# Optimization experiments

Measured on AMD Instinct MI355X. Metric: run time of the kernel, lower is better.

## Reference

```python
import jax, jax.numpy as jnp
import numpy as np

N, S, E, H = 8, 1024, 1024, 16
DK = E // H

def setup_inputs() -> dict:
    key = jax.random.key(0)
    ks = jax.random.split(key, 10)
    s = 1.0 / np.sqrt(E)
    x = jax.random.normal(ks[0], (N, S, E), dtype=jnp.float32)
    attn_mask = jax.random.randint(ks[1], (N, S, S), 0, 2) == 1
    Wq = jax.random.normal(ks[2], (E, E), dtype=jnp.float32) * s
    Wk = jax.random.normal(ks[3], (E, E), dtype=jnp.float32) * s
    Wv = jax.random.normal(ks[4], (E, E), dtype=jnp.float32) * s
    Wo = jax.random.normal(ks[5], (E, E), dtype=jnp.float32) * s
    bq = jax.random.normal(ks[6], (E,), dtype=jnp.float32) * s
    bk = jax.random.normal(ks[7], (E,), dtype=jnp.float32) * s
    bv = jax.random.normal(ks[8], (E,), dtype=jnp.float32) * s
    bo = jax.random.normal(ks[9], (E,), dtype=jnp.float32) * s
    return {"x": x, "attn_mask": attn_mask, "Wq": Wq, "bq": bq, "Wk": Wk, "bk": bk,
            "Wv": Wv, "bv": bv, "Wo": Wo, "bo": bo}

def reference(x, attn_mask, Wq, bq, Wk, bk, Wv, bv, Wo, bo):
    n, s, e = x.shape
    # projections, split into heads: (N, H, S, DK)
    q = (x @ Wq + bq).reshape(n, s, H, DK).transpose(0, 2, 1, 3)
    k = (x @ Wk + bk).reshape(n, s, H, DK).transpose(0, 2, 1, 3)
    v = (x @ Wv + bv).reshape(n, s, H, DK).transpose(0, 2, 1, 3)
    logits = jnp.einsum("nhqd,nhkd->nhqk", q, k) / np.sqrt(DK).astype(np.float32)
    # mask==True positions are suppressed (masked_fill with -1e9)
    logits = jnp.where(attn_mask[:, None, :, :], jnp.float32(-1e9), logits)
    attn = jax.nn.softmax(logits, axis=-1)  # exp(log_softmax) == softmax
    o = jnp.einsum("nhqk,nhkd->nhqd", attn, v)
    o = o.transpose(0, 2, 1, 3).reshape(n, s, e)
    return o @ Wo + bo
```

## Files before the change

### kernel.cpp

```cpp
#include <hip/hip_runtime.h>
#include <hip/hip_bf16.h>

typedef unsigned short u16;
typedef unsigned int   u32;
typedef unsigned long long u64;

#define SEQ 1024
#define EMB 1024
#define NH  16
#define DKH 64

#define QSCALE 0.18033688f

typedef __attribute__((ext_vector_type(8))) short short8;
typedef __attribute__((ext_vector_type(4))) float floatx4;

__device__ __forceinline__ float b2f(u16 u) {
  return __uint_as_float(((u32)u) << 16);
}
__device__ __forceinline__ u16 f2b(float f) {
  u32 u = __float_as_uint(f);
  u32 r = u + 0x7fffu + ((u >> 16) & 1u);
  return (u16)(r >> 16);
}

__device__ __forceinline__ void glds16(const u16* g, u16* l) {
  __builtin_amdgcn_global_load_lds(
      (const __attribute__((address_space(1))) u32*)g,
      (__attribute__((address_space(3))) u32*)l, 16, 0, 0);
}

__global__ __launch_bounds__(256) void probe_inputs(const u32* __restrict__ A,
                                                    const u32* __restrict__ B,
                                                    int* __restrict__ flags) {
  __shared__ int mA, mB, mBig, xB16;
  if (threadIdx.x == 0) { mA = 0; mB = 0; mBig = 0; xB16 = 0; }
  __syncthreads();
  int la = 0, lb = 0;
  for (int i = threadIdx.x; i < 4096; i += 256) {
    if ((A[i] & 0xFEFEFEFEu) == 0) la++;
    if ((B[i] & 0xFEFEFEFEu) == 0) lb++;
  }
  atomicAdd(&mA, la); atomicAdd(&mB, lb);
  __syncthreads();
  const int xIsB = (mA > mB) ? 1 : 0;
  const u32* X = xIsB ? B : A;
  const u32* M = xIsB ? A : B;
  int big = 0, cnt = 0;
  for (int i = threadIdx.x; i < 4096; i += 256)
    if (M[i] > 1u) big = 1;
  for (int i = threadIdx.x; i < 2048; i += 256) {
    u16 v = (u16)(X[i] & 0xffffu);
    int e = (v >> 7) & 0xFF;
    if (e >= 110 && e <= 135) cnt++;
  }
  if (big) atomicOr(&mBig, 1);
  atomicAdd(&xB16, cnt);
  __syncthreads();
  if (threadIdx.x == 0) {
    flags[0] = xIsB;
    flags[1] = (xB16 > 1500) ? 1 : 0;
    flags[2] = mBig;
  }
}

__global__ __launch_bounds__(256) void convert_x(const void* __restrict__ bigA,
                                                 const void* __restrict__ bigB,
                                                 const int* __restrict__ flags,
                                                 u16* __restrict__ out) {
  const void* x = flags[0] ? bigB : bigA;
  int i = (blockIdx.x * 256 + threadIdx.x) * 4;
  if (flags[1]) {
    *(ushort4*)(out + i) = *(const ushort4*)((const u16*)x + i);
  } else {
    float4 v = *(const float4*)((const float*)x + i);
    ushort4 o;
    o.x = f2b(v.x); o.y = f2b(v.y); o.z = f2b(v.z); o.w = f2b(v.w);
    *(ushort4*)(out + i) = o;
  }
}

__global__ __launch_bounds__(256) void build_maskbits(const void* __restrict__ bigA,
                                                      const void* __restrict__ bigB,
                                                      const int* __restrict__ flags,
                                                      u32* __restrict__ out) {
  const void* mask = flags[0] ? bigA : bigB;
  const int mbyte = flags[2];
  const int t = threadIdx.x;
  const int lane = t & 63, w = t >> 6;
  const u64 base0 = (u64)blockIdx.x * 8192;
#pragma unroll 4
  for (int k = 0; k < 32; k++) {
    u64 idx = base0 + k * 256 + t;
    int v;
    if (mbyte) v = ((const unsigned char*)mask)[idx] == 0;
    else       v = ((const u32*)mask)[idx] == 0;
    u64 b = __ballot(v);
    if (lane == 0) {
      u64 wbase = (base0 + k * 256 + w * 64) >> 5;
      out[wbase]     = (u32)b;
      out[wbase + 1] = (u32)(b >> 32);
    }
  }
}

__global__ __launch_bounds__(256) void transpose_convert_w4(
    const void* __restrict__ w0, const void* __restrict__ w1,
    const void* __restrict__ w2, const void* __restrict__ w3,
    u16* __restrict__ outQKV, u16* __restrict__ outO,
    const int* __restrict__ flags) {
  __shared__ float tile[32][33];
  const int z = blockIdx.z;
  const void* in = (z == 0) ? w0 : (z == 1) ? w1 : (z == 2) ? w2 : w3;
  u16* out = (z < 3) ? (outQKV + (u64)z * EMB * EMB) : outO;
  const float scale = (z == 0) ? QSCALE : 1.0f;
  const int amode = flags[1];
  const int tx = threadIdx.x & 31;
  const int ty = threadIdx.x >> 5;
  const int bx = blockIdx.x * 32, by = blockIdx.y * 32;
  if (amode) {
    const u16* inb = (const u16*)in;
#pragma unroll
    for (int r = ty; r < 32; r += 8)
      tile[r][tx] = b2f(inb[(u64)(by + r) * EMB + bx + tx]);
  } else {
    const float* inf = (const float*)in;
#pragma unroll
    for (int r = ty; r < 32; r += 8)
      tile[r][tx] = inf[(u64)(by + r) * EMB + bx + tx];
  }
  __syncthreads();
#pragma unroll
  for (int r = ty; r < 32; r += 8)
    out[(u64)(bx + r) * EMB + by + tx] = f2b(tile[tx][r] * scale);
}

__global__ __launch_bounds__(256) void convert_biases(const void* b0, const void* b1,
                                                      const void* b2, const void* b3,
                                                      float* __restrict__ out,
                                                      const int* __restrict__ flags) {
  const void* ptrs[4] = {b0, b1, b2, b3};
  const void* p = ptrs[blockIdx.x];
  const float scale = (blockIdx.x == 0) ? QSCALE : 1.0f;
  const int amode = flags[1];
  for (int i = threadIdx.x; i < 1024; i += 256) {
    float v = amode ? b2f(((const u16*)p)[i]) : ((const float*)p)[i];
    out[blockIdx.x * 1024 + i] = v * scale;
  }
}


template <int OUTMODE>
__device__ __forceinline__ void gemm_core(
    const u16* __restrict__ X, const u16* __restrict__ Wt,
    const float* __restrict__ bias,
    u16* __restrict__ Qg, u16* __restrict__ Kg, u16* __restrict__ Vt,
    float* __restrict__ outf, int row0) {
  __shared__ __align__(16) u16 lds[2][(256 + 128) * 64];
  const int t = threadIdx.x;
  const int lane = t & 63;
  const int w = t >> 6;
  const int wr = w >> 1, wc = w & 1;
  const int l15 = lane & 15, l4 = lane >> 4;
  const int bM = blockIdx.x * 256, bN = blockIdx.y * 128;
  const int r7 = l15 & 7;
  const int cA = (l4 ^ r7) << 3;
  const int cB = (l4 ^ r7 ^ 4) << 3;

  floatx4 acc[4][4];
#pragma unroll
  for (int i = 0; i < 4; i++)
#pragma unroll
    for (int j = 0; j < 4; j++)
      acc[i][j] = (floatx4){0.f, 0.f, 0.f, 0.f};

  const int srow = w * 8 + (lane >> 3);
  const int schk = ((lane & 7) ^ (lane >> 3)) << 3;
  const u16* Ap = X + (u64)(row0 + bM + srow) * EMB + schk;
  const u16* Bp = Wt + (u64)(bN + srow) * EMB + schk;
  u16* Ad0 = &lds[0][w * 512];
  u16* Bd0 = &lds[0][16384 + w * 512];
  u16* Ad1 = &lds[1][w * 512];
  u16* Bd1 = &lds[1][16384 + w * 512];

  auto stage = [&](u16* Ad, u16* Bd, int k0) {
    glds16(Ap + k0, Ad);
    glds16(Ap + k0 + 64 * EMB, Ad + 4096);
    glds16(Ap + k0 + 128 * EMB, Ad + 8192);
    glds16(Ap + k0 + 192 * EMB, Ad + 12288);
    glds16(Bp + k0, Bd);
    glds16(Bp + k0 + 64 * EMB, Bd + 4096);
  };

  auto compute = [&](const u16* __restrict__ Ab, const u16* __restrict__ Bb) {
    short8 bf[4][2];
#pragma unroll
    for (int n = 0; n < 4; n++) {
      const int gr = (wc * 64 + n * 16 + l15) * 64;
      bf[n][0] = *(const short8*)(&Bb[gr + cA]);
      bf[n][1] = *(const short8*)(&Bb[gr + cB]);
    }
#pragma unroll
    for (int mh = 0; mh < 2; mh++) {
      short8 af[2][2];
#pragma unroll
      for (int m = 0; m < 2; m++) {
        const int fr = (wr * 64 + mh * 32 + m * 16 + l15) * 64;
        af[m][0] = *(const short8*)(&Ab[fr + cA]);
        af[m][1] = *(const short8*)(&Ab[fr + cB]);
      }
      __builtin_amdgcn_s_setprio(1);
#pragma unroll
      for (int m = 0; m < 2; m++)
#pragma unroll
        for (int n = 0; n < 4; n++) {
          acc[mh * 2 + m][n] = __builtin_amdgcn_mfma_f32_16x16x32_bf16(
              af[m][0], bf[n][0], acc[mh * 2 + m][n], 0, 0, 0);
          acc[mh * 2 + m][n] = __builtin_amdgcn_mfma_f32_16x16x32_bf16(
              af[m][1], bf[n][1], acc[mh * 2 + m][n], 0, 0, 0);
        }
      __builtin_amdgcn_s_setprio(0);
    }
  };

  stage(Ad0, Bd0, 0);
  for (int k0 = 0; k0 < EMB; k0 += 128) {
    stage(Ad1, Bd1, k0 + 64);
    asm volatile("s_waitcnt vmcnt(6)" ::: "memory");
    asm volatile("s_barrier" ::: "memory");
    compute(&lds[0][0], &lds[0][16384]);
    asm volatile("s_barrier" ::: "memory");
    if (k0 + 128 < EMB) {
      stage(Ad0, Bd0, k0 + 128);
      asm volatile("s_waitcnt vmcnt(6)" ::: "memory");
    } else {
      asm volatile("s_waitcnt vmcnt(0)" ::: "memory");
    }
    asm volatile("s_barrier" ::: "memory");
    compute(&lds[1][0], &lds[1][16384]);
    asm volatile("s_barrier" ::: "memory");
  }

  if (OUTMODE == 0) {
    const int sec = bN >> 10;
    if (sec < 2) {
      u16* outp = (sec == 0) ? Qg : Kg;
#pragma unroll
      for (int n = 0; n < 4; n++) {
        int col = bN + wc * 64 + n * 16 + l15;
        float bv = bias[col];
        int colh = col & 1023;
        int h = colh >> 6, d = colh & 63;
#pragma unroll
        for (int mt = 0; mt < 4; mt++) {
#pragma unroll
          for (int r = 0; r < 4; r++) {
            int row = bM + wr * 64 + mt * 16 + l4 * 4 + r;
            float v = acc[mt][n][r] + bv;
            int nb = row >> 10, s = row & 1023;
            outp[((u64)((nb * NH + h) * SEQ + s)) * DKH + d] = f2b(v);
          }
        }
      }
    } else {
      u16* ldt = &lds[0][0];
#pragma unroll
      for (int n = 0; n < 4; n++) {
        const int dl = wc * 64 + n * 16 + l15;
        const float bv = bias[bN + dl];
#pragma unroll
        for (int mt = 0; mt < 4; mt++) {
          const int sb = wr * 64 + mt * 16 + l4 * 4;
          const int sp = sb ^ ((dl & 7) << 3);
          u32 w0 = (u32)f2b(acc[mt][n][0] + bv) |
                   ((u32)f2b(acc[mt][n][1] + bv) << 16);
          u32 w1 = (u32)f2b(acc[mt][n][2] + bv) |
                   ((u32)f2b(acc[mt][n][3] + bv) << 16);
          *(u32*)(&ldt[dl * 256 + sp])     = w0;
          *(u32*)(&ldt[dl * 256 + sp + 2]) = w1;
        }
      }
      __syncthreads();
      const int d  = t >> 2;
      const int sq = (t & 3) * 64;
      const int arow = row0 + bM;
      const int nb = arow >> 10, s0 = arow & 1023;
      const int h = ((bN & 1023) >> 6) + (d >> 6);
      u16* vout = Vt + (u64)(nb * NH + h) * SEQ * DKH +
                  (u64)(d & 63) * SEQ + s0 + sq;
#pragma unroll
      for (int c = 0; c < 8; c++) {
        const int sc = sq + c * 8;
        const int scs = sc ^ ((d & 7) << 3);
        *(uint4*)(vout + c * 8) = *(const uint4*)(&ldt[d * 256 + scs]);
      }
    }
  } else {
#pragma unroll
    for (int n = 0; n < 4; n++) {
      int col = bN + wc * 64 + n * 16 + l15;
      float bv = bias[col];
#pragma unroll
      for (int mt = 0; mt < 4; mt++) {
#pragma unroll
        for (int r = 0; r < 4; r++) {
          int row = bM + wr * 64 + mt * 16 + l4 * 4 + r;
          outf[(u64)row * EMB + col] = acc[mt][n][r] + bv;
        }
      }
    }
  }
}

__global__ __launch_bounds__(512, 2) void gemm_qkv(
    const u16* __restrict__ X, const u16* __restrict__ Wt,
    const float* __restrict__ bias,
    u16* __restrict__ Qg, u16* __restrict__ Kg, u16* __restrict__ Vt,
    int row0) {
  gemm_core<0>(X, Wt, bias, Qg, Kg, Vt, nullptr, row0);
}

__global__ __launch_bounds__(512, 2) void gemm_out(
    const u16* __restrict__ X, const u16* __restrict__ Wt,
    const float* __restrict__ bias, float* __restrict__ out) {
  gemm_core<1>(X, Wt, bias, nullptr, nullptr, nullptr, out, 0);
}

__global__ __launch_bounds__(512, 4) void attn_mfma(
    const u16* __restrict__ Q, const u16* __restrict__ K,
    const u16* __restrict__ Vt, const u32* __restrict__ maskbits,
    int b0, u16* __restrict__ ctx) {
  __shared__ __align__(16) u16 Ks[2][64 * 64];
  __shared__ __align__(16) u16 Vs[64 * 64];
  __shared__ __align__(16) u16 Ps[256 * 64];

  const int t = threadIdx.x;
  const int lane = t & 63, w = t >> 6;
  const int l15 = lane & 15, l4 = lane >> 4;
  const int bid = blockIdx.x;
  const int h = bid & 15;
  const int qt = (bid >> 4) & 3;
  const int n = bid >> 6;
  const int nh = n * NH + h;
  const int q0 = qt * 256;
  const u64 hoff = (u64)nh * SEQ * DKH;

  const int r7 = l15 & 7;
  const int cA = (l4 ^ r7) << 3;
  const int cB = (l4 ^ r7 ^ 4) << 3;

  const int rt = w * 8 + (lane >> 3);
  const int chk = ((lane & 7) ^ (lane >> 3)) << 3;
  const u16* Kp = K + hoff + (u64)rt * DKH + chk;
  const u16* Vp = Vt + hoff + (u64)rt * SEQ + chk;
  const int ldsO = w * 512;

  short8 qf[2][2];
  {
    const u16* qpA = Q + hoff + (u64)(q0 + w * 32 + l15) * DKH + l4 * 8;
    qf[0][0] = *(const short8*)(qpA);
    qf[0][1] = *(const short8*)(qpA + 32);
    const u16* qpB = qpA + 16 * DKH;
    qf[1][0] = *(const short8*)(qpB);
    qf[1][1] = *(const short8*)(qpB + 32);
  }

  short8 ones;
#pragma unroll
  for (int e = 0; e < 8; e++) ones[e] = (short)0x3F80;

  floatx4 o[2][4];
#pragma unroll
  for (int s = 0; s < 2; s++)
#pragma unroll
    for (int j = 0; j < 4; j++) o[s][j] = (floatx4){0.f, 0.f, 0.f, 0.f};
  floatx4 osum[2];
  osum[0] = (floatx4){0.f, 0.f, 0.f, 0.f};
  osum[1] = (floatx4){0.f, 0.f, 0.f, 0.f};

  const u64 mrow0 = ((u64)((b0 + n) * SEQ + q0 + w * 32 + l15)) * 32;
  const u64 mrow1 = mrow0 + 16 * 32;
  const int pq0 = w * 32 + l15;
  const int pq1 = pq0 + 16;
  const int pc0 = (l4 * 4) ^ (r7 << 3);

  glds16(Kp, &Ks[0][ldsO]);
  glds16(Vp, &Vs[ldsO]);
  __syncthreads();

  int cur = 0;
  for (int kc = 0; kc < SEQ; kc += 64) {
    if (kc > 0) glds16(Vp + kc, &Vs[ldsO]);
    const int havek = (kc + 64 < SEQ);
    if (havek) glds16(Kp + (kc + 64) * DKH, &Ks[cur ^ 1][ldsO]);

    const u64 mb0 = *(const u64*)(maskbits + mrow0 + (kc >> 5));
    const u64 mb1 = *(const u64*)(maskbits + mrow1 + (kc >> 5));
    const u16* Kc = &Ks[cur][0];

    __builtin_amdgcn_s_setprio(1);
#pragma unroll
    for (int j = 0; j < 4; j++) {
      const int rb = (j * 16 + l15) * 64;
      short8 kb0 = *(const short8*)(&Kc[rb + cA]);
      short8 kb1 = *(const short8*)(&Kc[rb + cB]);
      floatx4 s0 = (floatx4){0.f, 0.f, 0.f, 0.f};
      floatx4 s1 = (floatx4){0.f, 0.f, 0.f, 0.f};
      s0 = __builtin_amdgcn_mfma_f32_16x16x32_bf16(kb0, qf[0][0], s0, 0, 0, 0);
      s0 = __builtin_amdgcn_mfma_f32_16x16x32_bf16(kb1, qf[0][1], s0, 0, 0, 0);
      s1 = __builtin_amdgcn_mfma_f32_16x16x32_bf16(kb0, qf[1][0], s1, 0, 0, 0);
      s1 = __builtin_amdgcn_mfma_f32_16x16x32_bf16(kb1, qf[1][1], s1, 0, 0, 0);

      const u32 mj0 = (u32)(mb0 >> (j * 16 + l4 * 4));
      const u32 mj1 = (u32)(mb1 >> (j * 16 + l4 * 4));
      float p00 = __uint_as_float(
          __float_as_uint(__builtin_amdgcn_exp2f(s0[0])) &
          (u32)__builtin_amdgcn_sbfe(mj0, 0, 1));
      float p01 = __uint_as_float(
          __float_as_uint(__builtin_amdgcn_exp2f(s0[1])) &
          (u32)__builtin_amdgcn_sbfe(mj0, 1, 1));
      float p02 = __uint_as_float(
          __float_as_uint(__builtin_amdgcn_exp2f(s0[2])) &
          (u32)__builtin_amdgcn_sbfe(mj0, 2, 1));
      float p03 = __uint_as_float(
          __float_as_uint(__builtin_amdgcn_exp2f(s0[3])) &
          (u32)__builtin_amdgcn_sbfe(mj0, 3, 1));
      float p10 = __uint_as_float(
          __float_as_uint(__builtin_amdgcn_exp2f(s1[0])) &
          (u32)__builtin_amdgcn_sbfe(mj1, 0, 1));
      float p11 = __uint_as_float(
          __float_as_uint(__builtin_amdgcn_exp2f(s1[1])) &
          (u32)__builtin_amdgcn_sbfe(mj1, 1, 1));
      float p12 = __uint_as_float(
          __float_as_uint(__builtin_amdgcn_exp2f(s1[2])) &
          (u32)__builtin_amdgcn_sbfe(mj1, 2, 1));
      float p13 = __uint_as_float(
          __float_as_uint(__builtin_amdgcn_exp2f(s1[3])) &
          (u32)__builtin_amdgcn_sbfe(mj1, 3, 1));

      uint2 pk0, pk1;
      asm("v_cvt_pk_bf16_f32 %0, %1, %2" : "=v"(pk0.x) : "v"(p00), "v"(p01));
      asm("v_cvt_pk_bf16_f32 %0, %1, %2" : "=v"(pk0.y) : "v"(p02), "v"(p03));
      asm("v_cvt_pk_bf16_f32 %0, %1, %2" : "=v"(pk1.x) : "v"(p10), "v"(p11));
      asm("v_cvt_pk_bf16_f32 %0, %1, %2" : "=v"(pk1.y) : "v"(p12), "v"(p13));
      const int pcol = (j * 16) ^ pc0;
      *(uint2*)(&Ps[pq0 * 64 + pcol]) = pk0;
      *(uint2*)(&Ps[pq1 * 64 + pcol]) = pk1;
    }

    if (havek) asm volatile("s_waitcnt vmcnt(1)" ::: "memory");
    else       asm volatile("s_waitcnt vmcnt(0)" ::: "memory");
    __builtin_amdgcn_s_barrier();

    short8 pa[2][2];
    pa[0][0] = *(const short8*)(&Ps[pq0 * 64 + cA]);
    pa[0][1] = *(const short8*)(&Ps[pq0 * 64 + cB]);
    pa[1][0] = *(const short8*)(&Ps[pq1 * 64 + cA]);
    pa[1][1] = *(const short8*)(&Ps[pq1 * 64 + cB]);
#pragma unroll
    for (int j = 0; j < 4; j++) {
      const int rb = (j * 16 + l15) * 64;
      short8 vb0 = *(const short8*)(&Vs[rb + cA]);
      short8 vb1 = *(const short8*)(&Vs[rb + cB]);
      o[0][j] = __builtin_amdgcn_mfma_f32_16x16x32_bf16(pa[0][0], vb0, o[0][j], 0, 0, 0);
      o[0][j] = __builtin_amdgcn_mfma_f32_16x16x32_bf16(pa[0][1], vb1, o[0][j], 0, 0, 0);
      o[1][j] = __builtin_amdgcn_mfma_f32_16x16x32_bf16(pa[1][0], vb0, o[1][j], 0, 0, 0);
      o[1][j] = __builtin_amdgcn_mfma_f32_16x16x32_bf16(pa[1][1], vb1, o[1][j], 0, 0, 0);
    }
    osum[0] = __builtin_amdgcn_mfma_f32_16x16x32_bf16(pa[0][0], ones, osum[0], 0, 0, 0);
    osum[0] = __builtin_amdgcn_mfma_f32_16x16x32_bf16(pa[0][1], ones, osum[0], 0, 0, 0);
    osum[1] = __builtin_amdgcn_mfma_f32_16x16x32_bf16(pa[1][0], ones, osum[1], 0, 0, 0);
    osum[1] = __builtin_amdgcn_mfma_f32_16x16x32_bf16(pa[1][1], ones, osum[1], 0, 0, 0);
    __builtin_amdgcn_s_setprio(0);

    __syncthreads();
    cur ^= 1;
  }

#pragma unroll
  for (int s = 0; s < 2; s++) {
#pragma unroll
    for (int r = 0; r < 4; r++) {
      float invr = 1.0f / fmaxf(osum[s][r], 1e-30f);
      int q = q0 + w * 32 + s * 16 + l4 * 4 + r;
      u64 base = ((u64)(n * SEQ + q)) * EMB + h * DKH + l15;
#pragma unroll
      for (int j = 0; j < 4; j++)
        ctx[base + j * 16] = f2b(o[s][j][r] * invr);
    }
  }
}

extern "C" void kernel_launch(void* const* d_in, const int* in_sizes, int n_in,
                              void* d_out, int out_size, void* d_ws, size_t ws_size,
                              hipStream_t stream) {
  int bigI[2] = {0, 1}, wI[4] = {2, 4, 6, 8}, bI[4] = {3, 5, 7, 9};
  int nb = 0, nw = 0, nbi = 0;
  for (int i = 0; i < n_in; i++) {
    if (in_sizes[i] == 8388608) { if (nb < 2) bigI[nb++] = i; }
    else if (in_sizes[i] == 1048576) { if (nw < 4) wI[nw++] = i; }
    else if (in_sizes[i] == 1024) { if (nbi < 4) bI[nbi++] = i; }
  }
  int oq = 0, ok = 1, ov = 2, oo = 3;
  if (nb == 2 && bigI[0] == 4 && bigI[1] == 9) { oq = 2; ok = 0; ov = 3; oo = 1; }

  const void* bigA = d_in[bigI[0]];
  const void* bigB = d_in[bigI[1]];
  const void* Wq = d_in[wI[oq]];
  const void* Wk = d_in[wI[ok]];
  const void* Wv = d_in[wI[ov]];
  const void* Wo = d_in[wI[oo]];
  const void* bq = d_in[bI[oq]];
  const void* bk = d_in[bI[ok]];
  const void* bv = d_in[bI[ov]];
  const void* bo = d_in[bI[oo]];

  char* ws = (char*)d_ws;
  u16* WtQKV = (u16*)ws;
  u16* WtO   = (u16*)(ws + (6ull << 20));
  float* biasf = (float*)(ws + (8ull << 20));
  int* flags = (int*)(ws + (8ull << 20) + 16384);
  u32* maskbits = (u32*)(ws + (8ull << 20) + 65536);
  u16* xb = (u16*)(ws + (10ull << 20));
  char* grp = ws + (26ull << 20);

  int G = 1;
  for (int g = 8; g >= 1; g >>= 1) {
    if (ws_size >= (26ull << 20) + (u64)g * (8ull << 20)) { G = g; break; }
  }
  const u64 gsz = (u64)G * (2ull << 20);
  u16* Qg = (u16*)grp;
  u16* Kg = (u16*)(grp + gsz);
  u16* ctx = (u16*)(grp + 2 * gsz);
  u16* Vt = (u16*)(grp + 3 * gsz);

  dim3 tb(256);

  probe_inputs<<<dim3(1), tb, 0, stream>>>((const u32*)bigA, (const u32*)bigB, flags);
  convert_x<<<dim3(8192), tb, 0, stream>>>(bigA, bigB, flags, xb);
  build_maskbits<<<dim3(1024), tb, 0, stream>>>(bigA, bigB, flags, maskbits);

  transpose_convert_w4<<<dim3(32, 32, 4), tb, 0, stream>>>(Wq, Wk, Wv, Wo, WtQKV, WtO, flags);
  convert_biases<<<dim3(4), tb, 0, stream>>>(bq, bk, bv, bo, biasf, flags);

  for (int b0 = 0; b0 < 8; b0 += G) {
    int row0 = b0 * 1024;
    gemm_qkv<<<dim3(4 * G, 24), dim3(512), 0, stream>>>(xb, WtQKV, biasf, Qg, Kg, Vt, row0);

    attn_mfma<<<dim3(G * 16 * 4), dim3(512), 0, stream>>>(Qg, Kg, Vt, maskbits, b0, ctx);

    gemm_out<<<dim3(4 * G, 8), dim3(512), 0, stream>>>(ctx, WtO, biasf + 3072,
                                                       (float*)d_out + (u64)row0 * EMB);
  }
}
```

Before: 304.4 us.

## Triple-buffer GEMM LDS and interleave prefetch loads with MFMA phases

Replaces the double-buffered K loop in the shared projection GEMM with a three-stage LDS ring, prefetching two tiles ahead. Each iteration splits its work into four MFMA phases separated by barriers, and the global-to-LDS loads for the next stage are spread across those phases. The intent is to hide global memory latency better and to keep MFMA issue dense while loads are in flight. In exchange it uses 50% more LDS, which can lower occupancy, and adds more barriers per iteration.

```diff
diff --git a/kernel.cpp b/kernel.cpp
--- a/kernel.cpp
+++ b/kernel.cpp
@@ -14,6 +14,8 @@
 
 typedef __attribute__((ext_vector_type(8))) short short8;
 typedef __attribute__((ext_vector_type(4))) float floatx4;
+
+#define MM(A, B, C) C = __builtin_amdgcn_mfma_f32_16x16x32_bf16(A, B, C, 0, 0, 0)
 
 __device__ __forceinline__ float b2f(u16 u) {
   return __uint_as_float(((u32)u) << 16);
@@ -150,13 +152,15 @@
 }
 
 
+#define LDSB 24576
+
 template <int OUTMODE>
 __device__ __forceinline__ void gemm_core(
     const u16* __restrict__ X, const u16* __restrict__ Wt,
     const float* __restrict__ bias,
     u16* __restrict__ Qg, u16* __restrict__ Kg, u16* __restrict__ Vt,
     float* __restrict__ outf, int row0) {
-  __shared__ __align__(16) u16 lds[2][(256 + 128) * 64];
+  __shared__ __align__(16) u16 lds[3 * LDSB];
   const int t = threadIdx.x;
   const int lane = t & 63;
   const int w = t >> 6;
@@ -178,67 +182,103 @@
   const int schk = ((lane & 7) ^ (lane >> 3)) << 3;
   const u16* Ap = X + (u64)(row0 + bM + srow) * EMB + schk;
   const u16* Bp = Wt + (u64)(bN + srow) * EMB + schk;
-  u16* Ad0 = &lds[0][w * 512];
-  u16* Bd0 = &lds[0][16384 + w * 512];
-  u16* Ad1 = &lds[1][w * 512];
-  u16* Bd1 = &lds[1][16384 + w * 512];
-
-  auto stage = [&](u16* Ad, u16* Bd, int k0) {
+  const int wo = w * 512;
+
+#pragma unroll
+  for (int b = 0; b < 2; b++) {
+    u16* Ad = lds + b * LDSB + wo;
+    u16* Bd = lds + b * LDSB + 16384 + wo;
+    const int k0 = b * 64;
     glds16(Ap + k0, Ad);
     glds16(Ap + k0 + 64 * EMB, Ad + 4096);
     glds16(Ap + k0 + 128 * EMB, Ad + 8192);
     glds16(Ap + k0 + 192 * EMB, Ad + 12288);
     glds16(Bp + k0, Bd);
     glds16(Bp + k0 + 64 * EMB, Bd + 4096);
-  };
-
-  auto compute = [&](const u16* __restrict__ Ab, const u16* __restrict__ Bb) {
-    short8 bf[4][2];
-#pragma unroll
-    for (int n = 0; n < 4; n++) {
-      const int gr = (wc * 64 + n * 16 + l15) * 64;
-      bf[n][0] = *(const short8*)(&Bb[gr + cA]);
-      bf[n][1] = *(const short8*)(&Bb[gr + cB]);
-    }
-#pragma unroll
-    for (int mh = 0; mh < 2; mh++) {
-      short8 af[2][2];
-#pragma unroll
-      for (int m = 0; m < 2; m++) {
-        const int fr = (wr * 64 + mh * 32 + m * 16 + l15) * 64;
-        af[m][0] = *(const short8*)(&Ab[fr + cA]);
-        af[m][1] = *(const short8*)(&Ab[fr + cB]);
-      }
-      __builtin_amdgcn_s_setprio(1);
-#pragma unroll
-      for (int m = 0; m < 2; m++)
-#pragma unroll
-        for (int n = 0; n < 4; n++) {
-          acc[mh * 2 + m][n] = __builtin_amdgcn_mfma_f32_16x16x32_bf16(
-              af[m][0], bf[n][0], acc[mh * 2 + m][n], 0, 0, 0);
-          acc[mh * 2 + m][n] = __builtin_amdgcn_mfma_f32_16x16x32_bf16(
-              af[m][1], bf[n][1], acc[mh * 2 + m][n], 0, 0, 0);
-        }
-      __builtin_amdgcn_s_setprio(0);
-    }
-  };
-
-  stage(Ad0, Bd0, 0);
-  for (int k0 = 0; k0 < EMB; k0 += 128) {
-    stage(Ad1, Bd1, k0 + 64);
-    asm volatile("s_waitcnt vmcnt(6)" ::: "memory");
-    asm volatile("s_barrier" ::: "memory");
-    compute(&lds[0][0], &lds[0][16384]);
-    asm volatile("s_barrier" ::: "memory");
-    if (k0 + 128 < EMB) {
-      stage(Ad0, Bd0, k0 + 128);
-      asm volatile("s_waitcnt vmcnt(6)" ::: "memory");
-    } else {
-      asm volatile("s_waitcnt vmcnt(0)" ::: "memory");
-    }
-    asm volatile("s_barrier" ::: "memory");
-    compute(&lds[1][0], &lds[1][16384]);
-    asm volatile("s_barrier" ::: "memory");
+  }
+  asm volatile("s_waitcnt vmcnt(6)" ::: "memory");
+  __builtin_amdgcn_s_barrier();
+
+  int cur = 0;
+#pragma unroll 1
+  for (int kt = 0; kt < 16; kt++) {
+    const u16* Ab = lds + cur * LDSB;
+    const u16* Bb = Ab + 16384;
+    const int nxb = (cur + 2 >= 3) ? (cur - 1) : (cur + 2);
+    u16* And = lds + nxb * LDSB + wo;
+    u16* Bnd = And + 16384;
+    const int kof = (kt + 2) * 64;
+    const bool pf = kt < 14;
+
+    short8 af[2][2], bf[4][2];
+    const int raA = (wr * 64 + l15) * 64;
+    const int rbB = (wc * 64 + l15) * 64;
+
+    af[0][0] = *(const short8*)&Ab[raA + cA];
+    af[0][1] = *(const short8*)&Ab[raA + cB];
+    af[1][0] = *(const short8*)&Ab[raA + 1024 + cA];
+    af[1][1] = *(const short8*)&Ab[raA + 1024 + cB];
+    bf[0][0] = *(const short8*)&Bb[rbB + cA];
+    bf[0][1] = *(const short8*)&Bb[rbB + cB];
+    bf[1][0] = *(const short8*)&Bb[rbB + 1024 + cA];
+    bf[1][1] = *(const short8*)&Bb[rbB + 1024 + cB];
+    if (pf) {
+      glds16(Ap + kof, And);
+      glds16(Ap + kof + 64 * EMB, And + 4096);
+    }
+    __builtin_amdgcn_s_barrier();
+    __builtin_amdgcn_s_setprio(1);
+    MM(af[0][0], bf[0][0], acc[0][0]); MM(af[0][1], bf[0][1], acc[0][0]);
+    MM(af[0][0], bf[1][0], acc[0][1]); MM(af[0][1], bf[1][1], acc[0][1]);
+    MM(af[1][0], bf[0][0], acc[1][0]); MM(af[1][1], bf[0][1], acc[1][0]);
+    MM(af[1][0], bf[1][0], acc[1][1]); MM(af[1][1], bf[1][1], acc[1][1]);
+    __builtin_amdgcn_s_setprio(0);
+    __builtin_amdgcn_s_barrier();
+
+    bf[2][0] = *(const short8*)&Bb[rbB + 2048 + cA];
+    bf[2][1] = *(const short8*)&Bb[rbB + 2048 + cB];
+    bf[3][0] = *(const short8*)&Bb[rbB + 3072 + cA];
+    bf[3][1] = *(const short8*)&Bb[rbB + 3072 + cB];
+    if (pf) {
+      glds16(Ap + kof + 128 * EMB, And + 8192);
+      glds16(Ap + kof + 192 * EMB, And + 12288);
+    }
+    __builtin_amdgcn_s_barrier();
+    __builtin_amdgcn_s_setprio(1);
+    MM(af[0][0], bf[2][0], acc[0][2]); MM(af[0][1], bf[2][1], acc[0][2]);
+    MM(af[0][0], bf[3][0], acc[0][3]); MM(af[0][1], bf[3][1], acc[0][3]);
+    MM(af[1][0], bf[2][0], acc[1][2]); MM(af[1][1], bf[2][1], acc[1][2]);
+    MM(af[1][0], bf[3][0], acc[1][3]); MM(af[1][1], bf[3][1], acc[1][3]);
+    __builtin_amdgcn_s_setprio(0);
+    __builtin_amdgcn_s_barrier();
+
+    af[0][0] = *(const short8*)&Ab[raA + 2048 + cA];
+    af[0][1] = *(const short8*)&Ab[raA + 2048 + cB];
+    af[1][0] = *(const short8*)&Ab[raA + 3072 + cA];
+    af[1][1] = *(const short8*)&Ab[raA + 3072 + cB];
+    if (pf) glds16(Bp + kof, Bnd);
+    __builtin_amdgcn_s_barrier();
+    __builtin_amdgcn_s_setprio(1);
+    MM(af[0][0], bf[2][0], acc[2][2]); MM(af[0][1], bf[2][1], acc[2][2]);
+    MM(af[0][0], bf[3][0], acc[2][3]); MM(af[0][1], bf[3][1], acc[2][3]);
+    MM(af[1][0], bf[2][0], acc[3][2]); MM(af[1][1], bf[2][1], acc[3][2]);
+    MM(af[1][0], bf[3][0], acc[3][3]); MM(af[1][1], bf[3][1], acc[3][3]);
+    __builtin_amdgcn_s_setprio(0);
+    __builtin_amdgcn_s_barrier();
+
+    if (pf) glds16(Bp + kof + 64 * EMB, Bnd + 4096);
+    __builtin_amdgcn_s_barrier();
+    __builtin_amdgcn_s_setprio(1);
+    MM(af[0][0], bf[0][0], acc[2][0]); MM(af[0][1], bf[0][1], acc[2][0]);
+    MM(af[0][0], bf[1][0], acc[2][1]); MM(af[0][1], bf[1][1], acc[2][1]);
+    MM(af[1][0], bf[0][0], acc[3][0]); MM(af[1][1], bf[0][1], acc[3][0]);
+    MM(af[1][0], bf[1][0], acc[3][1]); MM(af[1][1], bf[1][1], acc[3][1]);
+    __builtin_amdgcn_s_setprio(0);
+    if (kt < 14) asm volatile("s_waitcnt vmcnt(6)" ::: "memory");
+    else         asm volatile("s_waitcnt vmcnt(0)" ::: "memory");
+    __builtin_amdgcn_s_barrier();
+
+    cur = (cur == 2) ? 0 : cur + 1;
   }
 
   if (OUTMODE == 0) {
@@ -263,7 +303,7 @@
         }
       }
     } else {
-      u16* ldt = &lds[0][0];
+      u16* ldt = &lds[0];
 #pragma unroll
       for (int n = 0; n < 4; n++) {
         const int dl = wc * 64 + n * 16 + l15;
```

Result: no change. 309.0 us (+1.5%).

## Use 256x256 tiles with staggered interleaved prefetch in QKV projection GEMM

Applied to the files above, without the earlier changes.

Splits the QKV GEMM out of the shared template and gives it a 256x256 output tile per block (8 waves in a 2x4 layout, 8x4 accumulators per wave) instead of 256x128, halving the grid's N dimension. Global-to-LDS loads for the next k-tiles are spread across the four sub-steps of each k-iteration, with barriers between them, so loads overlap the MFMA work. The aim is more data reuse per LDS byte and fewer redundant A-tile reloads. The cost is higher register pressure from 128 accumulator floats and a fuller 128KB LDS buffer, which may lower occupancy. The V transpose epilogue is rewritten to match the larger tile.

```diff
diff --git a/kernel.cpp b/kernel.cpp
--- a/kernel.cpp
+++ b/kernel.cpp
@@ -14,6 +14,8 @@
 
 typedef __attribute__((ext_vector_type(8))) short short8;
 typedef __attribute__((ext_vector_type(4))) float floatx4;
+
+#define MM(A, B, C) C = __builtin_amdgcn_mfma_f32_16x16x32_bf16(A, B, C, 0, 0, 0)
 
 __device__ __forceinline__ float b2f(u16 u) {
   return __uint_as_float(((u32)u) << 16);
@@ -149,13 +151,171 @@
   }
 }
 
-
-template <int OUTMODE>
-__device__ __forceinline__ void gemm_core(
+__global__ __launch_bounds__(512, 2) void gemm_qkv(
     const u16* __restrict__ X, const u16* __restrict__ Wt,
     const float* __restrict__ bias,
     u16* __restrict__ Qg, u16* __restrict__ Kg, u16* __restrict__ Vt,
-    float* __restrict__ outf, int row0) {
+    int row0) {
+  __shared__ __align__(16) u16 lds[65536];
+  const int t = threadIdx.x;
+  const int lane = t & 63;
+  const int w = t >> 6;
+  const int wr = w >> 2, wc = w & 3;
+  const int l15 = lane & 15, l4 = lane >> 4;
+  const int bM = blockIdx.x * 256, bN = blockIdx.y * 256;
+  const int r7 = l15 & 7;
+  const int cA = (l4 ^ r7) << 3;
+  const int cB = (l4 ^ r7 ^ 4) << 3;
+
+  floatx4 acc[8][4];
+#pragma unroll
+  for (int i = 0; i < 8; i++)
+#pragma unroll
+    for (int j = 0; j < 4; j++)
+      acc[i][j] = (floatx4){0.f, 0.f, 0.f, 0.f};
+
+  const int srow = w * 8 + (lane >> 3);
+  const int schk = ((lane & 7) ^ (lane >> 3)) << 3;
+  const u16* Ap = X + (u64)(row0 + bM + srow) * EMB + schk;
+  const u16* Bp = Wt + (u64)(bN + srow) * EMB + schk;
+  const int wo = w * 512;
+
+#define STA(buf, g, kt) glds16(Ap + (g) * 64 * EMB + (kt) * 64, lds + (buf) * 32768 + (g) * 4096 + wo)
+#define STB(buf, g, kt) glds16(Bp + (g) * 64 * EMB + (kt) * 64, lds + (buf) * 32768 + 16384 + (g) * 4096 + wo)
+
+  STB(0, 0, 0); STB(0, 1, 0);
+  STB(0, 2, 0); STB(0, 3, 0);
+  STA(0, 0, 0); STA(0, 2, 0);
+  STA(0, 1, 0); STA(0, 3, 0);
+  STB(1, 0, 1); STB(1, 1, 1);
+  STB(1, 2, 1); STB(1, 3, 1);
+  STA(1, 0, 1); STA(1, 2, 1);
+  asm volatile("s_waitcnt vmcnt(6)" ::: "memory");
+  __builtin_amdgcn_s_barrier();
+
+#pragma unroll 1
+  for (int kt = 0; kt < 16; kt++) {
+    const int cur = kt & 1, nxt = cur ^ 1;
+    const u16* Ab = lds + cur * 32768;
+    const u16* Bb = Ab + 16384;
+    const int raA = (wr * 128 + l15) * 64;
+    const int rbB = (wc * 64 + l15) * 64;
+    short8 bf[4][2];
+    short8 af[2][2];
+
+    {
+#pragma unroll
+      for (int n = 0; n < 4; n++) {
+        bf[n][0] = *(const short8*)&Bb[rbB + n * 1024 + cA];
+        bf[n][1] = *(const short8*)&Bb[rbB + n * 1024 + cB];
+      }
+      af[0][0] = *(const short8*)&Ab[raA + cA];
+      af[0][1] = *(const short8*)&Ab[raA + cB];
+      af[1][0] = *(const short8*)&Ab[raA + 1024 + cA];
+      af[1][1] = *(const short8*)&Ab[raA + 1024 + cB];
+      if (kt + 1 < 16) { STA(nxt, 1, kt + 1); STA(nxt, 3, kt + 1); }
+      __builtin_amdgcn_s_barrier();
+      __builtin_amdgcn_s_setprio(1);
+#pragma unroll
+      for (int m = 0; m < 2; m++)
+#pragma unroll
+        for (int n = 0; n < 4; n++) {
+          MM(af[m][0], bf[n][0], acc[m][n]);
+          MM(af[m][1], bf[n][1], acc[m][n]);
+        }
+      __builtin_amdgcn_s_setprio(0);
+      __builtin_amdgcn_s_barrier();
+    }
+#pragma unroll
+    for (int q = 1; q < 4; q++) {
+      af[0][0] = *(const short8*)&Ab[raA + (2 * q) * 1024 + cA];
+      af[0][1] = *(const short8*)&Ab[raA + (2 * q) * 1024 + cB];
+      af[1][0] = *(const short8*)&Ab[raA + (2 * q + 1) * 1024 + cA];
+      af[1][1] = *(const short8*)&Ab[raA + (2 * q + 1) * 1024 + cB];
+      if (kt + 2 < 16) {
+        if (q == 1)      { STB(cur, 0, kt + 2); STB(cur, 1, kt + 2); }
+        else if (q == 2) { STB(cur, 2, kt + 2); STB(cur, 3, kt + 2); }
+        else             { STA(cur, 0, kt + 2); STA(cur, 2, kt + 2); }
+      }
+      __builtin_amdgcn_s_barrier();
+      __builtin_amdgcn_s_setprio(1);
+#pragma unroll
+      for (int m = 0; m < 2; m++)
+#pragma unroll
+        for (int n = 0; n < 4; n++) {
+          MM(af[m][0], bf[n][0], acc[2 * q + m][n]);
+          MM(af[m][1], bf[n][1], acc[2 * q + m][n]);
+        }
+      __builtin_amdgcn_s_setprio(0);
+      if (q == 3) {
+        if (kt < 14) asm volatile("s_waitcnt vmcnt(6)" ::: "memory");
+        else         asm volatile("s_waitcnt vmcnt(0)" ::: "memory");
+      }
+      __builtin_amdgcn_s_barrier();
+    }
+  }
+#undef STA
+#undef STB
+
+  const int sec = bN >> 10;
+  if (sec < 2) {
+    u16* outp = (sec == 0) ? Qg : Kg;
+#pragma unroll
+    for (int n = 0; n < 4; n++) {
+      int col = bN + wc * 64 + n * 16 + l15;
+      float bv = bias[col];
+      int colh = col & 1023;
+      int h = colh >> 6, d = colh & 63;
+#pragma unroll
+      for (int m = 0; m < 8; m++) {
+#pragma unroll
+        for (int r = 0; r < 4; r++) {
+          int row = bM + wr * 128 + m * 16 + l4 * 4 + r;
+          float v = acc[m][n][r] + bv;
+          int nb = row >> 10, s = row & 1023;
+          outp[((u64)((nb * NH + h) * SEQ + s)) * DKH + d] = f2b(v);
+        }
+      }
+    }
+  } else {
+    __syncthreads();
+    u16* ldt = &lds[0];
+#pragma unroll
+    for (int n = 0; n < 4; n++) {
+      const int dl = wc * 64 + n * 16 + l15;
+      const float bv = bias[bN + dl];
+#pragma unroll
+      for (int m = 0; m < 8; m++) {
+        const int sb = wr * 128 + m * 16 + l4 * 4;
+        const int sp = sb ^ ((dl & 7) << 3);
+        u32 w0 = (u32)f2b(acc[m][n][0] + bv) |
+                 ((u32)f2b(acc[m][n][1] + bv) << 16);
+        u32 w1 = (u32)f2b(acc[m][n][2] + bv) |
+                 ((u32)f2b(acc[m][n][3] + bv) << 16);
+        *(u32*)(&ldt[dl * 256 + sp])     = w0;
+        *(u32*)(&ldt[dl * 256 + sp + 2]) = w1;
+      }
+    }
+    __syncthreads();
+    const int d  = t >> 1;
+    const int sh = (t & 1) * 128;
+    const int arow = row0 + bM;
+    const int nb = arow >> 10, s0 = arow & 1023;
+    const int h = ((bN & 1023) >> 6) + (d >> 6);
+    u16* vout = Vt + (u64)(nb * NH + h) * SEQ * DKH +
+                (u64)(d & 63) * SEQ + s0 + sh;
+#pragma unroll
+    for (int c = 0; c < 16; c++) {
+      const int sc = sh + c * 8;
+      const int scs = sc ^ ((d & 7) << 3);
+      *(uint4*)(vout + c * 8) = *(const uint4*)(&ldt[d * 256 + scs]);
+    }
+  }
+}
+
+__global__ __launch_bounds__(512, 2) void gemm_out(
+    const u16* __restrict__ X, const u16* __restrict__ Wt,
+    const float* __restrict__ bias, float* __restrict__ out) {
   __shared__ __align__(16) u16 lds[2][(256 + 128) * 64];
   const int t = threadIdx.x;
   const int lane = t & 63;
@@ -176,7 +336,7 @@
 
   const int srow = w * 8 + (lane >> 3);
   const int schk = ((lane & 7) ^ (lane >> 3)) << 3;
-  const u16* Ap = X + (u64)(row0 + bM + srow) * EMB + schk;
+  const u16* Ap = X + (u64)(bM + srow) * EMB + schk;
   const u16* Bp = Wt + (u64)(bN + srow) * EMB + schk;
   u16* Ad0 = &lds[0][w * 512];
   u16* Bd0 = &lds[0][16384 + w * 512];
@@ -193,16 +353,15 @@
   };
 
   auto compute = [&](const u16* __restrict__ Ab, const u16* __restrict__ Bb) {
-    short8 bf[4][2];
+    short8 af[2][2], bfr[4][2];
 #pragma unroll
     for (int n = 0; n < 4; n++) {
       const int gr = (wc * 64 + n * 16 + l15) * 64;
-      bf[n][0] = *(const short8*)(&Bb[gr + cA]);
-      bf[n][1] = *(const short8*)(&Bb[gr + cB]);
+      bfr[n][0] = *(const short8*)(&Bb[gr + cA]);
+      bfr[n][1] = *(const short8*)(&Bb[gr + cB]);
     }
 #pragma unroll
     for (int mh = 0; mh < 2; mh++) {
-      short8 af[2][2];
 #pragma unroll
       for (int m = 0; m < 2; m++) {
         const int fr = (wr * 64 + mh * 32 + m * 16 + l15) * 64;
@@ -214,10 +373,8 @@
       for (int m = 0; m < 2; m++)
 #pragma unroll
         for (int n = 0; n < 4; n++) {
-          acc[mh * 2 + m][n] = __builtin_amdgcn_mfma_f32_16x16x32_bf16(
-              af[m][0], bf[n][0], acc[mh * 2 + m][n], 0, 0, 0);
-          acc[mh * 2 + m][n] = __builtin_amdgcn_mfma_f32_16x16x32_bf16(
-              af[m][1], bf[n][1], acc[mh * 2 + m][n], 0, 0, 0);
+          MM(af[m][0], bfr[n][0], acc[mh * 2 + m][n]);
+          MM(af[m][1], bfr[n][1], acc[mh * 2 + m][n]);
         }
       __builtin_amdgcn_s_setprio(0);
     }
@@ -241,89 +398,19 @@
     asm volatile("s_barrier" ::: "memory");
   }
 
-  if (OUTMODE == 0) {
-    const int sec = bN >> 10;
-    if (sec < 2) {
-      u16* outp = (sec == 0) ? Qg : Kg;
-#pragma unroll
-      for (int n = 0; n < 4; n++) {
-        int col = bN + wc * 64 + n * 16 + l15;
-        float bv = bias[col];
-        int colh = col & 1023;
-        int h = colh >> 6, d = colh & 63;
-#pragma unroll
-        for (int mt = 0; mt < 4; mt++) {
-#pragma unroll
-          for (int r = 0; r < 4; r++) {
-            int row = bM + wr * 64 + mt * 16 + l4 * 4 + r;
-            float v = acc[mt][n][r] + bv;
-            int nb = row >> 10, s = row & 1023;
-            outp[((u64)((nb * NH + h) * SEQ + s)) * DKH + d] = f2b(v);
-          }
-        }
+#pragma unroll
+  for (int n = 0; n < 4; n++) {
+    int col = bN + wc * 64 + n * 16 + l15;
+    float bv = bias[col];
+#pragma unroll
+    for (int mt = 0; mt < 4; mt++) {
+#pragma unroll
+      for (int r = 0; r < 4; r++) {
+        int row = bM + wr * 64 + mt * 16 + l4 * 4 + r;
+        out[(u64)row * EMB + col] = acc[mt][n][r] + bv;
       }
-    } else {
-      u16* ldt = &lds[0][0];
-#pragma unroll
-      for (int n = 0; n < 4; n++) {
-        const int dl = wc * 64 + n * 16 + l15;
-        const float bv = bias[bN + dl];
-#pragma unroll
-        for (int mt = 0; mt < 4; mt++) {
-          const int sb = wr * 64 + mt * 16 + l4 * 4;
-          const int sp = sb ^ ((dl & 7) << 3);
-          u32 w0 = (u32)f2b(acc[mt][n][0] + bv) |
-                   ((u32)f2b(acc[mt][n][1] + bv) << 16);
-          u32 w1 = (u32)f2b(acc[mt][n][2] + bv) |
-                   ((u32)f2b(acc[mt][n][3] + bv) << 16);
-          *(u32*)(&ldt[dl * 256 + sp])     = w0;
-          *(u32*)(&ldt[dl * 256 + sp + 2]) = w1;
-        }
-      }
-      __syncthreads();
-      const int d  = t >> 2;
-      const int sq = (t & 3) * 64;
-      const int arow = row0 + bM;
-      const int nb = arow >> 10, s0 = arow & 1023;
-      const int h = ((bN & 1023) >> 6) + (d >> 6);
-      u16* vout = Vt + (u64)(nb * NH + h) * SEQ * DKH +
-                  (u64)(d & 63) * SEQ + s0 + sq;
-#pragma unroll
-      for (int c = 0; c < 8; c++) {
-        const int sc = sq + c * 8;
-        const int scs = sc ^ ((d & 7) << 3);
-        *(uint4*)(vout + c * 8) = *(const uint4*)(&ldt[d * 256 + scs]);
-      }
-    }
-  } else {
-#pragma unroll
-    for (int n = 0; n < 4; n++) {
-      int col = bN + wc * 64 + n * 16 + l15;
-      float bv = bias[col];
-#pragma unroll
-      for (int mt = 0; mt < 4; mt++) {
-#pragma unroll
-        for (int r = 0; r < 4; r++) {
-          int row = bM + wr * 64 + mt * 16 + l4 * 4 + r;
-          outf[(u64)row * EMB + col] = acc[mt][n][r] + bv;
-        }
-      }
-    }
-  }
-}
-
-__global__ __launch_bounds__(512, 2) void gemm_qkv(
-    const u16* __restrict__ X, const u16* __restrict__ Wt,
-    const float* __restrict__ bias,
-    u16* __restrict__ Qg, u16* __restrict__ Kg, u16* __restrict__ Vt,
-    int row0) {
-  gemm_core<0>(X, Wt, bias, Qg, Kg, Vt, nullptr, row0);
-}
-
-__global__ __launch_bounds__(512, 2) void gemm_out(
-    const u16* __restrict__ X, const u16* __restrict__ Wt,
-    const float* __restrict__ bias, float* __restrict__ out) {
-  gemm_core<1>(X, Wt, bias, nullptr, nullptr, nullptr, out, 0);
+    }
+  }
 }
 
 __global__ __launch_bounds__(512, 4) void attn_mfma(
@@ -545,7 +632,7 @@
 
   for (int b0 = 0; b0 < 8; b0 += G) {
     int row0 = b0 * 1024;
-    gemm_qkv<<<dim3(4 * G, 24), dim3(512), 0, stream>>>(xb, WtQKV, biasf, Qg, Kg, Vt, row0);
+    gemm_qkv<<<dim3(4 * G, 12), dim3(512), 0, stream>>>(xb, WtQKV, biasf, Qg, Kg, Vt, row0);
 
     attn_mfma<<<dim3(G * 16 * 4), dim3(512), 0, stream>>>(Qg, Kg, Vt, maskbits, b0, ctx);
 
```

New measurement: 317.7 us. 4.4% more time.
